# Kernel tuning notes

Measured on AMD Instinct MI355X. Metric: run time of the kernel, lower is better.

Reference implementation:

```python
import jax, jax.numpy as jnp
import numpy as np
import math

S, B, F, D, H, L, DFF, PRED = 448, 64, 8, 256, 8, 4, 256, 96
DK = D // H
EPS = 1e-5


def _pos_enc(length, d_model):
    pos = jnp.arange(length, dtype=jnp.float32)[:, None]            # [S,1]
    div = jnp.exp(jnp.arange(0, d_model, 2, dtype=jnp.float32) * (-math.log(10000.0) / d_model))
    pe = jnp.zeros((length, d_model), jnp.float32)
    pe = pe.at[:, 0::2].set(jnp.sin(pos * div))
    pe = pe.at[:, 1::2].set(jnp.cos(pos * div))
    return pe[:, None, :]                                            # [S,1,D]


def _layernorm(x, g, b):
    mu = jnp.mean(x, axis=-1, keepdims=True)
    var = jnp.mean((x - mu) ** 2, axis=-1, keepdims=True)
    return (x - mu) / jnp.sqrt(var + EPS) * g + b


def setup_inputs() -> dict:
    key = jax.random.key(0)
    ks = jax.random.split(key, 12)
    g = lambda k, shape: (jax.random.normal(k, shape) * 0.02).astype(jnp.float32)
    return {
        "src": jax.random.normal(ks[0], (S, B, F), jnp.float32),
        "w_in": g(ks[1], (F, D)), "b_in": jnp.zeros((D,), jnp.float32),
        "Wq": g(ks[2], (L, D, D)), "bq": jnp.zeros((L, D), jnp.float32),
        "Wk": g(ks[3], (L, D, D)), "bk": jnp.zeros((L, D), jnp.float32),
        "Wv": g(ks[4], (L, D, D)), "bv": jnp.zeros((L, D), jnp.float32),
        "Wo": g(ks[5], (L, D, D)), "bo": jnp.zeros((L, D), jnp.float32),
        "g1": jnp.ones((L, D), jnp.float32), "be1": jnp.zeros((L, D), jnp.float32),
        "W1": g(ks[6], (L, D, DFF)), "b1": jnp.zeros((L, DFF), jnp.float32),
        "W2": g(ks[7], (L, DFF, D)), "b2": jnp.zeros((L, D), jnp.float32),
        "g2": jnp.ones((L, D), jnp.float32), "be2": jnp.zeros((L, D), jnp.float32),
        "w_out": g(ks[8], (D, F)), "b_out": jnp.zeros((F,), jnp.float32),
    }


def reference(src, w_in, b_in, Wq, bq, Wk, bk, Wv, bv, Wo, bo,
              g1, be1, W1, b1, W2, b2, g2, be2, w_out, b_out):
    x = src @ w_in + b_in                 # [S,B,D]
    x = x + _pos_enc(S, D)

    scale = math.sqrt(DK)

    def layer(x, p):
        wq, bq_, wk, bk_, wv, bv_, wo, bo_, g1_, be1_, w1, b1_, w2, b2_, g2_, be2_ = p
        Q = (x @ wq + bq_).reshape(S, B, H, DK)
        K = (x @ wk + bk_).reshape(S, B, H, DK)
        V = (x @ wv + bv_).reshape(S, B, H, DK)
        scores = jnp.einsum("sbhd,tbhd->bhst", Q, K) / scale   # [B,H,S,S]
        attn = jax.nn.softmax(scores, axis=-1)
        ctx = jnp.einsum("bhst,tbhd->sbhd", attn, V).reshape(S, B, D)
        x = _layernorm(x + (ctx @ wo + bo_), g1_, be1_)
        ff = jax.nn.relu(x @ w1 + b1_) @ w2 + b2_
        x = _layernorm(x + ff, g2_, be2_)
        return x, None

    x, _ = jax.lax.scan(layer, x, (Wq, bq, Wk, bk, Wv, bv, Wo, bo,
                                   g1, be1, W1, b1, W2, b2, g2, be2))
    return x[-PRED:] @ w_out + b_out      # [PRED,B,F]
```

## Files before the change

### kernel.cpp

```cpp
#include <hip/hip_runtime.h>
#include <hip/hip_bf16.h>
#include <math.h>

#define S_ 448
#define B_ 64
#define F_ 8
#define D_ 256
#define H_ 8
#define DK_ 32
#define L_ 4
#define PRED_ 96
#define NT_ (S_ * B_)
#define PANEL_ (S_ * DK_)
#define VTP_ (32 * 512)

typedef unsigned short bf16_t;
using bf16x8 = __attribute__((ext_vector_type(8))) short;
using f32x4  = __attribute__((ext_vector_type(4))) float;
using f32x16 = __attribute__((ext_vector_type(16))) float;

__device__ __forceinline__ float b2f(bf16_t b) {
  return __uint_as_float(((unsigned)b) << 16);
}
__device__ __forceinline__ bf16_t f2b(float f) {
  unsigned u = __float_as_uint(f);
  u += 0x7fffu + ((u >> 16) & 1u);
  return (bf16_t)(u >> 16);
}
__device__ __forceinline__ unsigned pk2(float lo, float hi) {
  union { __hip_bfloat162 h; unsigned u; } c;
  c.h = __float22bfloat162_rn(make_float2(lo, hi));
  return c.u;
}

__global__ __launch_bounds__(256) void embed_kernel(
    const float* __restrict__ src, const float* __restrict__ w_in,
    const float* __restrict__ b_in, bf16_t* __restrict__ x) {
  int n = blockIdx.x;
  int d = threadIdx.x;
  const float* srow = src + (size_t)n * F_;
  float acc = b_in[d];
#pragma unroll
  for (int f = 0; f < F_; ++f) acc += srow[f] * w_in[f * D_ + d];
  int s = n / B_;
  int i2 = d & ~1;
  float freq = __expf(-9.210340371976184f * (float)i2 / (float)D_);
  float ang = (float)s * freq;
  float pe = (d & 1) ? cosf(ang) : sinf(ang);
  x[(size_t)n * D_ + d] = f2b(acc + pe);
}

__global__ __launch_bounds__(256) void transpose_w_kernel(
    const float* __restrict__ W, bf16_t* __restrict__ Wt) {
  __shared__ float t[32][33];
  int l = blockIdx.z;
  int k0 = blockIdx.x * 32, n0 = blockIdx.y * 32;
  int x = threadIdx.x, y = threadIdx.y;
  const float* src = W + ((size_t)l * 256 + k0) * 256 + n0;
#pragma unroll
  for (int i = y; i < 32; i += 8) t[i][x] = src[(size_t)i * 256 + x];
  __syncthreads();
  bf16_t* dst = Wt + ((size_t)l * 256 + n0) * 256 + k0;
#pragma unroll
  for (int i = y; i < 32; i += 8) dst[(size_t)i * 256 + x] = f2b(t[x][i]);
}

__global__ __launch_bounds__(512) void vtrans_kernel(
    const bf16_t* __restrict__ V, bf16_t* __restrict__ Vt) {
  __shared__ bf16_t t[32][456];
  int bh = blockIdx.x, tid = threadIdx.x;
  const bf16_t* Vp = V + (size_t)bh * PANEL_;
#pragma unroll
  for (int p = 0; p < 4; ++p) {
    int idx = tid + p * 512;
    if (idx < 1792) {
      int s = idx >> 2, c = idx & 3;
      uint4 v = *(const uint4*)(Vp + s * 32 + c * 8);
      unsigned w[4] = {v.x, v.y, v.z, v.w};
#pragma unroll
      for (int e = 0; e < 8; ++e) {
        bf16_t val = (bf16_t)((e & 1) ? (w[e >> 1] >> 16) : (w[e >> 1] & 0xffff));
        *(bf16_t*)((char*)&t[0][0] + (c * 8 + e) * 912 + s * 2) = val;
      }
    }
  }
  __syncthreads();
  bf16_t* Op = Vt + (size_t)bh * VTP_;
#pragma unroll
  for (int p = 0; p < 4; ++p) {
    int idx = tid + p * 512;
    int dk = idx >> 6, sl = idx & 63;
    uint4 v = {0, 0, 0, 0};
    if (sl < 56) v = *(const uint4*)((char*)&t[0][0] + dk * 912 + sl * 16);
    *(uint4*)(Op + dk * 512 + sl * 8) = v;
  }
}

template <int ALAY, int OLAY, int RELU>
__device__ __forceinline__ void gemm_body(
    const bf16_t* __restrict__ A, const bf16_t* __restrict__ Wt,
    const float* __restrict__ bias, bf16_t* __restrict__ Y, int m0, int n0) {
  __shared__ bf16_t As[2][128][32];
  __shared__ bf16_t Bs[2][128][32];
  int tid = threadIdx.x, lane = tid & 63, wv = tid >> 6;
  int wr = wv >> 2, wc = wv & 3;
  int jg = lane >> 4, fr = lane & 15;
  int s_row = tid >> 2;
  int s_p = tid & 3;

  uint4 rA, rB;

  auto stage_load = [&](int kt) {
    int k0 = kt * 32;
    int ls = s_p ^ ((s_row >> 1) & 3);
    const bf16_t* ap;
    if (ALAY == 0) {
      ap = A + (size_t)(m0 + s_row) * 256 + k0 + ls * 8;
    } else {
      int n = m0 + s_row;
      int k = k0 + ls * 8;
      ap = A + ((size_t)(((n & 63) << 3) | (k >> 5)) * S_ + (n >> 6)) * DK_ +
           (k & 31);
    }
    rA = *(const uint4*)ap;
    rB = *(const uint4*)(Wt + (size_t)(n0 + s_row) * 256 + k0 + ls * 8);
  };
  auto stage_write = [&](int buf) {
    *(uint4*)(&As[buf][s_row][s_p * 8]) = rA;
    *(uint4*)(&Bs[buf][s_row][s_p * 8]) = rB;
  };

  f32x4 zero = {0.f, 0.f, 0.f, 0.f};
  f32x4 acc[4][2];
#pragma unroll
  for (int i = 0; i < 4; ++i)
#pragma unroll
    for (int j = 0; j < 2; ++j) acc[i][j] = zero;

  stage_load(0);
  stage_write(0);
  __syncthreads();

  for (int kt = 0; kt < 8; ++kt) {
    int buf = kt & 1;
    if (kt < 7) stage_load(kt + 1);
    bf16x8 af[4], bfr[2];
#pragma unroll
    for (int mi = 0; mi < 4; ++mi) {
      int row = wr * 64 + mi * 16 + fr;
      af[mi] = *(const bf16x8*)((const char*)&As[buf][0][0] + row * 64 +
                                ((jg ^ ((row >> 1) & 3)) << 4));
    }
#pragma unroll
    for (int ni = 0; ni < 2; ++ni) {
      int rn = wc * 32 + ni * 16 + fr;
      bfr[ni] = *(const bf16x8*)((const char*)&Bs[buf][0][0] + rn * 64 +
                                 ((jg ^ ((rn >> 1) & 3)) << 4));
    }
#pragma unroll
    for (int mi = 0; mi < 4; ++mi)
#pragma unroll
      for (int ni = 0; ni < 2; ++ni)
        acc[mi][ni] = __builtin_amdgcn_mfma_f32_16x16x32_bf16(
            af[mi], bfr[ni], acc[mi][ni], 0, 0, 0);
    if (kt < 7) {
      stage_write((kt + 1) & 1);
      __syncthreads();
    }
  }

  __syncthreads();
  char* ep0 = (char*)&As[0][0][0] + wv * 1024;
  float bcol[2];
#pragma unroll
  for (int ni = 0; ni < 2; ++ni) bcol[ni] = bias[n0 + wc * 32 + ni * 16 + fr];
#pragma unroll
  for (int mi = 0; mi < 4; ++mi) {
    char* ep = ep0 + (mi & 1) * 8192;
#pragma unroll
    for (int ni = 0; ni < 2; ++ni)
#pragma unroll
      for (int r = 0; r < 4; ++r) {
        float v = acc[mi][ni][r] + bcol[ni];
        if (RELU) v = fmaxf(v, 0.f);
        int row = jg * 4 + r;
        int cb = (ni * 16 + fr) * 2;
        *(bf16_t*)(ep + row * 64 + (cb ^ (jg << 4))) = f2b(v);
      }
    int row16 = lane >> 2, c = lane & 3;
    uint4 v = *(uint4*)(ep + row16 * 64 +
                        ((c << 4) ^ (((row16 >> 2) & 3) << 4)));
    int n = m0 + wr * 64 + mi * 16 + row16;
    if (OLAY == 0) {
      *(uint4*)((char*)(Y + (size_t)n * 256 + n0 + wc * 32) + c * 16) = v;
    } else {
      int h = (n0 + wc * 32) >> 5;
      *(uint4*)((char*)(Y + ((size_t)(((n & 63) << 3) | h) * S_ + (n >> 6)) *
                                DK_) +
                c * 16) = v;
    }
  }
}

__global__ __launch_bounds__(512, 4) void gemm_qkv_kernel(
    const bf16_t* __restrict__ A, const bf16_t* __restrict__ wq,
    const bf16_t* __restrict__ wk, const bf16_t* __restrict__ wvp,
    const float* __restrict__ bq, const float* __restrict__ bk,
    const float* __restrict__ bvp, bf16_t* __restrict__ yq,
    bf16_t* __restrict__ yk, bf16_t* __restrict__ yv) {
  int sel = blockIdx.y >> 1;
  const bf16_t* W = sel == 0 ? wq : sel == 1 ? wk : wvp;
  const float* bb = sel == 0 ? bq : sel == 1 ? bk : bvp;
  bf16_t* Y = sel == 0 ? yq : sel == 1 ? yk : yv;
  gemm_body<0, 1, 0>(A, W, bb, Y, blockIdx.x * 128, (blockIdx.y & 1) * 128);
}

__global__ __launch_bounds__(512, 4) void gemm_ctx_kernel(
    const bf16_t* __restrict__ A, const bf16_t* __restrict__ Wt,
    const float* __restrict__ bias, bf16_t* __restrict__ Y) {
  gemm_body<1, 0, 0>(A, Wt, bias, Y, blockIdx.x * 128, blockIdx.y * 128);
}
__global__ __launch_bounds__(512, 4) void gemm_relu_kernel(
    const bf16_t* __restrict__ A, const bf16_t* __restrict__ Wt,
    const float* __restrict__ bias, bf16_t* __restrict__ Y) {
  gemm_body<0, 0, 1>(A, Wt, bias, Y, blockIdx.x * 128, blockIdx.y * 128);
}
__global__ __launch_bounds__(512, 4) void gemm_plain_kernel(
    const bf16_t* __restrict__ A, const bf16_t* __restrict__ Wt,
    const float* __restrict__ bias, bf16_t* __restrict__ Y) {
  gemm_body<0, 0, 0>(A, Wt, bias, Y, blockIdx.x * 128, blockIdx.y * 128);
}

__global__ __launch_bounds__(448) void attn_v5_kernel(
    bf16_t* __restrict__ Q, const bf16_t* __restrict__ K,
    const bf16_t* __restrict__ Vt) {
  __shared__ char Ep[7][2560];
  int tid = threadIdx.x, lane = tid & 63, wv = tid >> 6;
  int bid = blockIdx.x;
  int xcd = bid & 7, j = bid >> 3;
  int bh = ((j >> 1) << 3) | xcd;
  int qt = (j & 1) * 7 + wv;
  int q0 = qt * 32;
  bf16_t* Qp = Q + (size_t)bh * PANEL_;
  const bf16_t* Kp = K + (size_t)bh * PANEL_;
  const bf16_t* Vp = Vt + (size_t)bh * VTP_;
  int lo31 = lane & 31, hi = lane >> 5;
  const float sc_c = 0.25503484f;
  const f32x16 z16 = {0.f, 0.f, 0.f, 0.f, 0.f, 0.f, 0.f, 0.f,
                      0.f, 0.f, 0.f, 0.f, 0.f, 0.f, 0.f, 0.f};

  bf16x8 qf0 = *(const bf16x8*)(Qp + (q0 + lo31) * 32 + hi * 8);
  bf16x8 qf1 = *(const bf16x8*)(Qp + (q0 + lo31) * 32 + 16 + hi * 8);

  float m_run = -3.0e38f, l_run = 0.f;
  f32x16 o = z16;

  for (int kc = 0; kc < 7; ++kc) {
    int t0 = kc * 64;
    f32x16 s0 = z16, s1 = z16;
    {
      const bf16_t* kr0 = Kp + (t0 + lo31) * 32 + hi * 8;
      const bf16_t* kr1 = Kp + (t0 + 32 + lo31) * 32 + hi * 8;
      bf16x8 ka0 = *(const bf16x8*)(kr0);
      bf16x8 ka1 = *(const bf16x8*)(kr0 + 16);
      bf16x8 kb0 = *(const bf16x8*)(kr1);
      bf16x8 kb1 = *(const bf16x8*)(kr1 + 16);
      __builtin_amdgcn_s_setprio(1);
      s0 = __builtin_amdgcn_mfma_f32_32x32x16_bf16(ka0, qf0, s0, 0, 0, 0);
      s0 = __builtin_amdgcn_mfma_f32_32x32x16_bf16(ka1, qf1, s0, 0, 0, 0);
      s1 = __builtin_amdgcn_mfma_f32_32x32x16_bf16(kb0, qf0, s1, 0, 0, 0);
      s1 = __builtin_amdgcn_mfma_f32_32x32x16_bf16(kb1, qf1, s1, 0, 0, 0);
      __builtin_amdgcn_s_setprio(0);
    }
    float cm = -3.0e38f;
#pragma unroll
    for (int r = 0; r < 16; ++r) cm = fmaxf(cm, fmaxf(s0[r], s1[r]));
    cm = fmaxf(cm, __shfl_xor(cm, 32));
    float m_new = fmaxf(m_run, cm);
    float scale = exp2f((m_run - m_new) * sc_c);
    float ls = 0.f;
#pragma unroll
    for (int r = 0; r < 16; ++r) {
      float p0 = exp2f((s0[r] - m_new) * sc_c);
      float p1 = exp2f((s1[r] - m_new) * sc_c);
      s0[r] = p0; s1[r] = p1;
      ls += p0 + p1;
    }
    ls += __shfl_xor(ls, 32);
    l_run = l_run * scale + ls;
    m_run = m_new;
#pragma unroll
    for (int r = 0; r < 16; ++r) o[r] *= scale;

#define PV_SUB(SV, RB, TOFF)                                                  \
    {                                                                         \
      unsigned a0 = pk2(SV[RB + 0], SV[RB + 1]);                              \
      unsigned a1 = pk2(SV[RB + 2], SV[RB + 3]);                              \
      unsigned b0 = pk2(SV[RB + 4], SV[RB + 5]);                              \
      unsigned b1 = pk2(SV[RB + 6], SV[RB + 7]);                              \
      unsigned xa0 = (unsigned)__shfl_xor((int)a0, 32);                       \
      unsigned xa1 = (unsigned)__shfl_xor((int)a1, 32);                       \
      unsigned xb0 = (unsigned)__shfl_xor((int)b0, 32);                       \
      unsigned xb1 = (unsigned)__shfl_xor((int)b1, 32);                       \
      union { unsigned u[4]; bf16x8 v; } pf;                                  \
      pf.u[0] = hi ? xb0 : a0;                                                \
      pf.u[1] = hi ? xb1 : a1;                                                \
      pf.u[2] = hi ? b0 : xa0;                                                \
      pf.u[3] = hi ? b1 : xa1;                                                \
      bf16x8 vf = *(const bf16x8*)(Vp + lo31 * 512 + (TOFF) + hi * 8);        \
      o = __builtin_amdgcn_mfma_f32_32x32x16_bf16(pf.v, vf, o, 0, 0, 0);      \
    }
    PV_SUB(s0, 0, t0)
    PV_SUB(s0, 8, t0 + 16)
    PV_SUB(s1, 0, t0 + 32)
    PV_SUB(s1, 8, t0 + 48)
#undef PV_SUB
  }

  float inv = 1.f / l_run;
  char* ep = &Ep[wv][0];
#pragma unroll
  for (int r = 0; r < 16; ++r) {
    int q = (r & 3) + 8 * (r >> 2) + 4 * hi;
    float iq = __shfl(inv, q);
    *(bf16_t*)(ep + q * 80 + lo31 * 2) = f2b(o[r] * iq);
  }
#pragma unroll
  for (int ps = 0; ps < 2; ++ps) {
    int row = ps * 16 + (lane >> 2), ch = lane & 3;
    uint4 v = *(uint4*)(ep + row * 80 + ch * 16);
    *(uint4*)(Qp + (q0 + row) * 32 + ch * 8) = v;
  }
}

__global__ __launch_bounds__(512) void attn_v3f_kernel(
    bf16_t* __restrict__ Q, const bf16_t* __restrict__ K,
    const bf16_t* __restrict__ Vsrc) {
  __shared__ bf16_t Vt[32][520];
  __shared__ char Pbuf[8][2048];
  int tid = threadIdx.x, lane = tid & 63, wv = tid >> 6;
  int bid = blockIdx.x;
  int bh = (bid & 7) | ((bid >> 5) << 3);
  int chunk = (bid >> 3) & 3;
  bf16_t* Qp = Q + (size_t)bh * PANEL_;
  const bf16_t* Kp = K + (size_t)bh * PANEL_;
  int jg = lane >> 4, fr = lane & 15;

  const bf16_t* Vp = Vsrc + (size_t)bh * PANEL_;
  for (int idx = tid; idx < 448 * 4; idx += 512) {
    int t = idx >> 2, c = idx & 3;
    uint4 vv = *(const uint4*)(Vp + t * 32 + c * 8);
    unsigned w[4] = {vv.x, vv.y, vv.z, vv.w};
#pragma unroll
    for (int e = 0; e < 8; ++e) {
      bf16_t val = (bf16_t)((e & 1) ? (w[e >> 1] >> 16) : (w[e >> 1] & 0xffff));
      *(bf16_t*)((char*)&Vt[0][0] + (c * 8 + e) * 1040 + t * 2) = val;
    }
  }
  __syncthreads();

  int q0 = chunk * 128 + wv * 16;
  if (q0 < S_) {
    const float sc_c = 0.25503484f;
    f32x4 zero = {0.f, 0.f, 0.f, 0.f};
    bf16x8 qf = *(const bf16x8*)(Qp + (q0 + fr) * 32 + jg * 8);
    f32x4 s2[28];
#pragma unroll
    for (int ct = 0; ct < 28; ++ct) {
      bf16x8 kf = *(const bf16x8*)(Kp + (ct * 16 + fr) * 32 + jg * 8);
      s2[ct] = __builtin_amdgcn_mfma_f32_16x16x32_bf16(kf, qf, zero, 0, 0, 0);
    }
    float m = s2[0][0];
#pragma unroll
    for (int ct = 0; ct < 28; ++ct)
#pragma unroll
      for (int r = 0; r < 4; ++r) m = fmaxf(m, s2[ct][r]);
    m = fmaxf(m, __shfl_xor(m, 16));
    m = fmaxf(m, __shfl_xor(m, 32));
    float l = 0.f;
#pragma unroll
    for (int ct = 0; ct < 28; ++ct)
#pragma unroll
      for (int r = 0; r < 4; ++r) {
        float p = exp2f((s2[ct][r] - m) * sc_c);
        s2[ct][r] = p;
        l += p;
      }
    l += __shfl_xor(l, 16);
    l += __shfl_xor(l, 32);
    float inv = 1.f / l;

    char* pb0 = &Pbuf[wv][0];
    f32x4 o[2] = {zero, zero};
#pragma unroll
    for (int c = 0; c < 14; ++c) {
      char* pb = pb0 + (c & 1) * 1024;
      uint2 w0, w1;
      w0.x = pk2(s2[2 * c][0], s2[2 * c][1]);
      w0.y = pk2(s2[2 * c][2], s2[2 * c][3]);
      w1.x = pk2(s2[2 * c + 1][0], s2[2 * c + 1][1]);
      w1.y = pk2(s2[2 * c + 1][2], s2[2 * c + 1][3]);
      *(uint2*)(pb + fr * 64 + 8 * jg) = w0;
      *(uint2*)(pb + fr * 64 + 32 + 8 * jg) = w1;
      bf16x8 pf = *(const bf16x8*)(pb + fr * 64 + jg * 16);
#pragma unroll
      for (int nt = 0; nt < 2; ++nt) {
        bf16x8 vf = *(const bf16x8*)((const char*)&Vt[0][0] +
                                     (nt * 16 + fr) * 1040 +
                                     (c * 32 + jg * 8) * 2);
        o[nt] = __builtin_amdgcn_mfma_f32_16x16x32_bf16(pf, vf, o[nt], 0, 0, 0);
      }
    }
    float invq[4];
#pragma unroll
    for (int r = 0; r < 4; ++r) invq[r] = __shfl(inv, jg * 4 + r);
#pragma unroll
    for (int nt = 0; nt < 2; ++nt)
#pragma unroll
      for (int r = 0; r < 4; ++r) {
        float v = o[nt][r] * invq[r];
        int row = jg * 4 + r;
        int cb = (nt * 16 + fr) * 2;
        *(bf16_t*)(pb0 + row * 64 + (cb ^ (jg << 4))) = f2b(v);
      }
    {
      int row16 = lane >> 2, c = lane & 3;
      uint4 v = *(uint4*)(pb0 + row16 * 64 +
                          ((c << 4) ^ (((row16 >> 2) & 3) << 4)));
      *(uint4*)(Qp + (q0 + row16) * 32 + c * 8) = v;
    }
  }
}

__global__ __launch_bounds__(256) void resid_ln_kernel(
    bf16_t* __restrict__ x, const bf16_t* __restrict__ y,
    const float* __restrict__ g, const float* __restrict__ be) {
  int wv = threadIdx.x >> 6, lane = threadIdx.x & 63;
  size_t n = (size_t)blockIdx.x * 4 + wv;
  size_t off = n * D_ + lane * 4;
  ushort4 xv = *(const ushort4*)(x + off);
  ushort4 yv = *(const ushort4*)(y + off);
  float v[4];
  v[0] = b2f(xv.x) + b2f(yv.x);
  v[1] = b2f(xv.y) + b2f(yv.y);
  v[2] = b2f(xv.z) + b2f(yv.z);
  v[3] = b2f(xv.w) + b2f(yv.w);
  float sm = v[0] + v[1] + v[2] + v[3];
#pragma unroll
  for (int o = 32; o; o >>= 1) sm += __shfl_xor(sm, o);
  float mean = sm * (1.f / 256.f);
  float c[4], s2 = 0.f;
#pragma unroll
  for (int i = 0; i < 4; ++i) { c[i] = v[i] - mean; s2 += c[i] * c[i]; }
#pragma unroll
  for (int o = 32; o; o >>= 1) s2 += __shfl_xor(s2, o);
  float var = s2 * (1.f / 256.f);
  float r = rsqrtf(var + 1e-5f);
  float4 gv = *(const float4*)(g + lane * 4);
  float4 bv = *(const float4*)(be + lane * 4);
  ushort4 ov;
  ov.x = f2b(c[0] * r * gv.x + bv.x);
  ov.y = f2b(c[1] * r * gv.y + bv.y);
  ov.z = f2b(c[2] * r * gv.z + bv.z);
  ov.w = f2b(c[3] * r * gv.w + bv.w);
  *(ushort4*)(x + off) = ov;
}

__global__ __launch_bounds__(256) void out_kernel(
    const bf16_t* __restrict__ x, const float* __restrict__ w_out,
    const float* __restrict__ b_out, float* __restrict__ out) {
  int idx = blockIdx.x * 256 + threadIdx.x;
  int f = idx & 7;
  int pb = idx >> 3;
  const bf16_t* xrow = x + ((size_t)(S_ - PRED_) * B_ + pb) * D_;
  float acc = b_out[f];
  for (int dd = 0; dd < D_; ++dd) acc += b2f(xrow[dd]) * w_out[dd * F_ + f];
  out[idx] = acc;
}

extern "C" void kernel_launch(void* const* d_in, const int* in_sizes, int n_in,
                              void* d_out, int out_size, void* d_ws, size_t ws_size,
                              hipStream_t stream) {
  const float* src  = (const float*)d_in[0];
  const float* w_in = (const float*)d_in[1];
  const float* b_in = (const float*)d_in[2];
  const float* Wq = (const float*)d_in[3];
  const float* bq = (const float*)d_in[4];
  const float* Wk = (const float*)d_in[5];
  const float* bk = (const float*)d_in[6];
  const float* Wv = (const float*)d_in[7];
  const float* bv = (const float*)d_in[8];
  const float* Wo = (const float*)d_in[9];
  const float* bo = (const float*)d_in[10];
  const float* g1 = (const float*)d_in[11];
  const float* be1 = (const float*)d_in[12];
  const float* W1 = (const float*)d_in[13];
  const float* b1 = (const float*)d_in[14];
  const float* W2 = (const float*)d_in[15];
  const float* b2 = (const float*)d_in[16];
  const float* g2 = (const float*)d_in[17];
  const float* be2 = (const float*)d_in[18];
  const float* w_out = (const float*)d_in[19];
  const float* b_out = (const float*)d_in[20];
  float* out = (float*)d_out;

  const size_t NTD = (size_t)NT_ * D_;
  bf16_t* xb = (bf16_t*)d_ws;
  bf16_t* qb = xb + NTD;
  bf16_t* kb = qb + NTD;
  bf16_t* vb = kb + NTD;
  bf16_t* wt = vb + NTD;
  const size_t WSZ = (size_t)L_ * 65536;
  bf16_t* wtq = wt;
  bf16_t* wtk = wtq + WSZ;
  bf16_t* wtv = wtk + WSZ;
  bf16_t* wto = wtv + WSZ;
  bf16_t* wt1 = wto + WSZ;
  bf16_t* wt2 = wt1 + WSZ;
  bf16_t* vtb = wt2 + WSZ;

  const size_t NEED = ((size_t)4 * NTD + 6 * WSZ + (size_t)512 * VTP_) * 2;
  const int use_vt = (ws_size >= NEED) ? 1 : 0;

  dim3 tb(32, 8), tg(8, 8, L_);
  transpose_w_kernel<<<tg, tb, 0, stream>>>(Wq, wtq);
  transpose_w_kernel<<<tg, tb, 0, stream>>>(Wk, wtk);
  transpose_w_kernel<<<tg, tb, 0, stream>>>(Wv, wtv);
  transpose_w_kernel<<<tg, tb, 0, stream>>>(Wo, wto);
  transpose_w_kernel<<<tg, tb, 0, stream>>>(W1, wt1);
  transpose_w_kernel<<<tg, tb, 0, stream>>>(W2, wt2);

  embed_kernel<<<NT_, 256, 0, stream>>>(src, w_in, b_in, xb);

  dim3 gg(224, 2);
  for (int l = 0; l < L_; ++l) {
    const size_t woff = (size_t)l * 65536;
    const size_t boff = (size_t)l * D_;
    gemm_qkv_kernel<<<dim3(224, 6), 512, 0, stream>>>(
        xb, wtq + woff, wtk + woff, wtv + woff, bq + boff, bk + boff,
        bv + boff, qb, kb, vb);
    if (use_vt) {
      vtrans_kernel<<<512, 512, 0, stream>>>(vb, vtb);
      attn_v5_kernel<<<1024, 448, 0, stream>>>(qb, kb, vtb);
    } else {
      attn_v3f_kernel<<<2048, 512, 0, stream>>>(qb, kb, vb);
    }
    gemm_ctx_kernel<<<gg, 512, 0, stream>>>(qb, wto + woff, bo + boff, kb);
    resid_ln_kernel<<<NT_ / 4, 256, 0, stream>>>(xb, kb, g1 + boff, be1 + boff);
    gemm_relu_kernel<<<gg, 512, 0, stream>>>(xb, wt1 + woff, b1 + boff, qb);
    gemm_plain_kernel<<<gg, 512, 0, stream>>>(qb, wt2 + woff, b2 + boff, kb);
    resid_ln_kernel<<<NT_ / 4, 256, 0, stream>>>(xb, kb, g2 + boff, be2 + boff);
  }

  out_kernel<<<(PRED_ * B_ * F_) / 256, 256, 0, stream>>>(xb, w_out, b_out, out);
}
```

Before: 573.0 us.

## Fuse output-projection and FFN2 GEMMs with residual LayerNorm; lazy softmax rescale

```diff
diff --git a/kernel.cpp b/kernel.cpp
--- a/kernel.cpp
+++ b/kernel.cpp
@@ -208,27 +208,180 @@
     const float* __restrict__ bq, const float* __restrict__ bk,
     const float* __restrict__ bvp, bf16_t* __restrict__ yq,
     bf16_t* __restrict__ yk, bf16_t* __restrict__ yv) {
-  int sel = blockIdx.y >> 1;
-  const bf16_t* W = sel == 0 ? wq : sel == 1 ? wk : wvp;
-  const float* bb = sel == 0 ? bq : sel == 1 ? bk : bvp;
-  bf16_t* Y = sel == 0 ? yq : sel == 1 ? yk : yv;
-  gemm_body<0, 1, 0>(A, W, bb, Y, blockIdx.x * 128, (blockIdx.y & 1) * 128);
-}
-
-__global__ __launch_bounds__(512, 4) void gemm_ctx_kernel(
-    const bf16_t* __restrict__ A, const bf16_t* __restrict__ Wt,
-    const float* __restrict__ bias, bf16_t* __restrict__ Y) {
-  gemm_body<1, 0, 0>(A, Wt, bias, Y, blockIdx.x * 128, blockIdx.y * 128);
-}
+  int bid = blockIdx.x;
+  int w = (bid & 7) * 168 + (bid >> 3);
+  int sel = w % 6;
+  int m0 = (w / 6) * 128;
+  int mtx = sel >> 1;
+  const bf16_t* W = mtx == 0 ? wq : mtx == 1 ? wk : wvp;
+  const float* bb = mtx == 0 ? bq : mtx == 1 ? bk : bvp;
+  bf16_t* Y = mtx == 0 ? yq : mtx == 1 ? yk : yv;
+  gemm_body<0, 1, 0>(A, W, bb, Y, m0, (sel & 1) * 128);
+}
+
 __global__ __launch_bounds__(512, 4) void gemm_relu_kernel(
     const bf16_t* __restrict__ A, const bf16_t* __restrict__ Wt,
     const float* __restrict__ bias, bf16_t* __restrict__ Y) {
-  gemm_body<0, 0, 1>(A, Wt, bias, Y, blockIdx.x * 128, blockIdx.y * 128);
-}
-__global__ __launch_bounds__(512, 4) void gemm_plain_kernel(
+  int bid = blockIdx.x;
+  int w = (bid & 7) * 56 + (bid >> 3);
+  gemm_body<0, 0, 1>(A, Wt, bias, Y, (w >> 1) * 128, (w & 1) * 128);
+}
+
+template <int ALAY>
+__global__ __launch_bounds__(512, 2) void gemm_ln_kernel(
     const bf16_t* __restrict__ A, const bf16_t* __restrict__ Wt,
-    const float* __restrict__ bias, bf16_t* __restrict__ Y) {
-  gemm_body<0, 0, 0>(A, Wt, bias, Y, blockIdx.x * 128, blockIdx.y * 128);
+    const float* __restrict__ bias, const float* __restrict__ g,
+    const float* __restrict__ be, bf16_t* __restrict__ x) {
+  __shared__ char smem[40960];
+  int tid = threadIdx.x, lane = tid & 63, wv = tid >> 6;
+  int wr = wv >> 2, wc = wv & 3;
+  int jg = lane >> 4, fr = lane & 15;
+  int bid = blockIdx.x;
+  int m0 = ((bid & 7) * 56 + (bid >> 3)) * 64;
+
+  uint4 rA, rB0, rB1;
+  auto stage_load = [&](int kt) {
+    int k0 = kt * 32;
+    if (tid < 256) {
+      int row = tid >> 2, p = tid & 3;
+      int ls = p ^ ((row >> 1) & 3);
+      const bf16_t* ap;
+      if (ALAY == 0) {
+        ap = A + (size_t)(m0 + row) * 256 + k0 + ls * 8;
+      } else {
+        int n = m0 + row;
+        int k = k0 + ls * 8;
+        ap = A + ((size_t)(((n & 63) << 3) | (k >> 5)) * S_ + (n >> 6)) * DK_ +
+             (k & 31);
+      }
+      rA = *(const uint4*)ap;
+    }
+    int p = tid & 3;
+    int r0 = tid >> 2, r1 = 128 + (tid >> 2);
+    rB0 = *(const uint4*)(Wt + (size_t)r0 * 256 + k0 + (p ^ ((r0 >> 1) & 3)) * 8);
+    rB1 = *(const uint4*)(Wt + (size_t)r1 * 256 + k0 + (p ^ ((r1 >> 1) & 3)) * 8);
+  };
+  auto stage_write = [&](int buf) {
+    if (tid < 256)
+      *(uint4*)(smem + buf * 4096 + (tid >> 2) * 64 + (tid & 3) * 16) = rA;
+    char* bb = smem + 8192 + buf * 16384;
+    *(uint4*)(bb + (tid >> 2) * 64 + (tid & 3) * 16) = rB0;
+    *(uint4*)(bb + (128 + (tid >> 2)) * 64 + (tid & 3) * 16) = rB1;
+  };
+
+  f32x4 zero = {0.f, 0.f, 0.f, 0.f};
+  f32x4 acc[2][4];
+#pragma unroll
+  for (int i = 0; i < 2; ++i)
+#pragma unroll
+    for (int j = 0; j < 4; ++j) acc[i][j] = zero;
+
+  stage_load(0);
+  stage_write(0);
+  __syncthreads();
+
+  for (int kt = 0; kt < 8; ++kt) {
+    int buf = kt & 1;
+    if (kt < 7) stage_load(kt + 1);
+    bf16x8 af[2], bfr[4];
+#pragma unroll
+    for (int mi = 0; mi < 2; ++mi) {
+      int row = wr * 32 + mi * 16 + fr;
+      af[mi] = *(const bf16x8*)(smem + buf * 4096 + row * 64 +
+                                ((jg ^ ((row >> 1) & 3)) << 4));
+    }
+#pragma unroll
+    for (int ni = 0; ni < 4; ++ni) {
+      int rn = wc * 64 + ni * 16 + fr;
+      bfr[ni] = *(const bf16x8*)(smem + 8192 + buf * 16384 + rn * 64 +
+                                 ((jg ^ ((rn >> 1) & 3)) << 4));
+    }
+#pragma unroll
+    for (int mi = 0; mi < 2; ++mi)
+#pragma unroll
+      for (int ni = 0; ni < 4; ++ni)
+        acc[mi][ni] = __builtin_amdgcn_mfma_f32_16x16x32_bf16(
+            af[mi], bfr[ni], acc[mi][ni], 0, 0, 0);
+    if (kt < 7) {
+      stage_write((kt + 1) & 1);
+      __syncthreads();
+    }
+  }
+
+  __syncthreads();
+  float* ssum = (float*)smem;
+  float* ssq  = (float*)(smem + 1024);
+  float* rowm = (float*)(smem + 2048);
+  float* rowr = (float*)(smem + 2304);
+
+  float bcol[4], gv[4], bev[4];
+#pragma unroll
+  for (int ni = 0; ni < 4; ++ni) {
+    int c = wc * 64 + ni * 16 + fr;
+    bcol[ni] = bias[c];
+    gv[ni] = g[c];
+    bev[ni] = be[c];
+  }
+#pragma unroll
+  for (int mi = 0; mi < 2; ++mi)
+#pragma unroll
+    for (int r = 0; r < 4; ++r) {
+      int row = wr * 32 + mi * 16 + jg * 4 + r;
+      size_t gbase = (size_t)(m0 + row) * 256 + wc * 64 + fr;
+      float s = 0.f, s2 = 0.f;
+#pragma unroll
+      for (int ni = 0; ni < 4; ++ni) {
+        float v = acc[mi][ni][r] + bcol[ni] + b2f(x[gbase + ni * 16]);
+        acc[mi][ni][r] = v;
+        s += v;
+        s2 += v * v;
+      }
+#pragma unroll
+      for (int off = 1; off <= 8; off <<= 1) {
+        s += __shfl_xor(s, off);
+        s2 += __shfl_xor(s2, off);
+      }
+      if (fr == 0) {
+        ssum[row * 4 + wc] = s;
+        ssq[row * 4 + wc] = s2;
+      }
+    }
+  __syncthreads();
+  if (tid < 64) {
+    float s = ssum[tid * 4] + ssum[tid * 4 + 1] + ssum[tid * 4 + 2] +
+              ssum[tid * 4 + 3];
+    float q = ssq[tid * 4] + ssq[tid * 4 + 1] + ssq[tid * 4 + 2] +
+              ssq[tid * 4 + 3];
+    float mean = s * (1.f / 256.f);
+    float var = q * (1.f / 256.f) - mean * mean;
+    rowm[tid] = mean;
+    rowr[tid] = rsqrtf(var + 1e-5f);
+  }
+  __syncthreads();
+  char* ep0 = smem + 8192 + wv * 2048;
+#pragma unroll
+  for (int mi = 0; mi < 2; ++mi) {
+    char* ep = ep0 + mi * 16384;
+#pragma unroll
+    for (int r = 0; r < 4; ++r) {
+      int row = wr * 32 + mi * 16 + jg * 4 + r;
+      float mean = rowm[row], rinv = rowr[row];
+#pragma unroll
+      for (int ni = 0; ni < 4; ++ni) {
+        float lnv = (acc[mi][ni][r] - mean) * rinv * gv[ni] + bev[ni];
+        int cb = (ni * 16 + fr) * 2;
+        *(bf16_t*)(ep + (jg * 4 + r) * 128 + (cb ^ (jg << 4))) = f2b(lnv);
+      }
+    }
+    int row16 = lane >> 2;
+#pragma unroll
+    for (int ps = 0; ps < 2; ++ps) {
+      int ch = (lane & 3) + ps * 4;
+      uint4 v = *(uint4*)(ep + row16 * 128 + ((ch * 16) ^ ((row16 >> 2) << 4)));
+      *(uint4*)(x + (size_t)(m0 + wr * 32 + mi * 16 + row16) * 256 + wc * 64 +
+                ch * 8) = v;
+    }
+  }
 }
 
 __global__ __launch_bounds__(448) void attn_v5_kernel(
@@ -276,21 +429,24 @@
 #pragma unroll
     for (int r = 0; r < 16; ++r) cm = fmaxf(cm, fmaxf(s0[r], s1[r]));
     cm = fmaxf(cm, __shfl_xor(cm, 32));
-    float m_new = fmaxf(m_run, cm);
-    float scale = exp2f((m_run - m_new) * sc_c);
+    if (!__all(cm <= m_run + 16.0f)) {
+      float m_new = fmaxf(m_run, cm);
+      float scale = exp2f((m_run - m_new) * sc_c);
+      l_run *= scale;
+#pragma unroll
+      for (int r = 0; r < 16; ++r) o[r] *= scale;
+      m_run = m_new;
+    }
     float ls = 0.f;
 #pragma unroll
     for (int r = 0; r < 16; ++r) {
-      float p0 = exp2f((s0[r] - m_new) * sc_c);
-      float p1 = exp2f((s1[r] - m_new) * sc_c);
+      float p0 = exp2f((s0[r] - m_run) * sc_c);
+      float p1 = exp2f((s1[r] - m_run) * sc_c);
       s0[r] = p0; s1[r] = p1;
       ls += p0 + p1;
     }
     ls += __shfl_xor(ls, 32);
-    l_run = l_run * scale + ls;
-    m_run = m_new;
-#pragma unroll
-    for (int r = 0; r < 16; ++r) o[r] *= scale;
+    l_run += ls;
 
 #define PV_SUB(SV, RB, TOFF)                                                  \
     {                                                                         \
@@ -430,40 +586,6 @@
       *(uint4*)(Qp + (q0 + row16) * 32 + c * 8) = v;
     }
   }
-}
-
-__global__ __launch_bounds__(256) void resid_ln_kernel(
-    bf16_t* __restrict__ x, const bf16_t* __restrict__ y,
-    const float* __restrict__ g, const float* __restrict__ be) {
-  int wv = threadIdx.x >> 6, lane = threadIdx.x & 63;
-  size_t n = (size_t)blockIdx.x * 4 + wv;
-  size_t off = n * D_ + lane * 4;
-  ushort4 xv = *(const ushort4*)(x + off);
-  ushort4 yv = *(const ushort4*)(y + off);
-  float v[4];
-  v[0] = b2f(xv.x) + b2f(yv.x);
-  v[1] = b2f(xv.y) + b2f(yv.y);
-  v[2] = b2f(xv.z) + b2f(yv.z);
-  v[3] = b2f(xv.w) + b2f(yv.w);
-  float sm = v[0] + v[1] + v[2] + v[3];
-#pragma unroll
-  for (int o = 32; o; o >>= 1) sm += __shfl_xor(sm, o);
-  float mean = sm * (1.f / 256.f);
-  float c[4], s2 = 0.f;
-#pragma unroll
-  for (int i = 0; i < 4; ++i) { c[i] = v[i] - mean; s2 += c[i] * c[i]; }
-#pragma unroll
-  for (int o = 32; o; o >>= 1) s2 += __shfl_xor(s2, o);
-  float var = s2 * (1.f / 256.f);
-  float r = rsqrtf(var + 1e-5f);
-  float4 gv = *(const float4*)(g + lane * 4);
-  float4 bv = *(const float4*)(be + lane * 4);
-  ushort4 ov;
-  ov.x = f2b(c[0] * r * gv.x + bv.x);
-  ov.y = f2b(c[1] * r * gv.y + bv.y);
-  ov.z = f2b(c[2] * r * gv.z + bv.z);
-  ov.w = f2b(c[3] * r * gv.w + bv.w);
-  *(ushort4*)(x + off) = ov;
 }
 
 __global__ __launch_bounds__(256) void out_kernel(
@@ -532,11 +654,10 @@
 
   embed_kernel<<<NT_, 256, 0, stream>>>(src, w_in, b_in, xb);
 
-  dim3 gg(224, 2);
   for (int l = 0; l < L_; ++l) {
     const size_t woff = (size_t)l * 65536;
     const size_t boff = (size_t)l * D_;
-    gemm_qkv_kernel<<<dim3(224, 6), 512, 0, stream>>>(
+    gemm_qkv_kernel<<<1344, 512, 0, stream>>>(
         xb, wtq + woff, wtk + woff, wtv + woff, bq + boff, bk + boff,
         bv + boff, qb, kb, vb);
     if (use_vt) {
@@ -545,11 +666,11 @@
     } else {
       attn_v3f_kernel<<<2048, 512, 0, stream>>>(qb, kb, vb);
     }
-    gemm_ctx_kernel<<<gg, 512, 0, stream>>>(qb, wto + woff, bo + boff, kb);
-    resid_ln_kernel<<<NT_ / 4, 256, 0, stream>>>(xb, kb, g1 + boff, be1 + boff);
-    gemm_relu_kernel<<<gg, 512, 0, stream>>>(xb, wt1 + woff, b1 + boff, qb);
-    gemm_plain_kernel<<<gg, 512, 0, stream>>>(qb, wt2 + woff, b2 + boff, kb);
-    resid_ln_kernel<<<NT_ / 4, 256, 0, stream>>>(xb, kb, g2 + boff, be2 + boff);
+    gemm_ln_kernel<1><<<448, 512, 0, stream>>>(qb, wto + woff, bo + boff,
+                                               g1 + boff, be1 + boff, xb);
+    gemm_relu_kernel<<<448, 512, 0, stream>>>(xb, wt1 + woff, b1 + boff, qb);
+    gemm_ln_kernel<0><<<448, 512, 0, stream>>>(qb, wt2 + woff, b2 + boff,
+                                               g2 + boff, be2 + boff, xb);
   }
 
   out_kernel<<<(PRED_ * B_ * F_) / 256, 256, 0, stream>>>(xb, w_out, b_out, out);
```

Result: faster. 536.3 us (-6.4%).
